# Kernel tuning notes

Hardware: AMD Instinct MI355X
Metric: run time of the kernel (lower is better)

Reference implementation:

```python
import jax, jax.numpy as jnp
import numpy as np

B, L, H, E = 8, 1024, 8, 64
HIST = 512


def setup_inputs() -> dict:
    key = jax.random.key(0)
    ks = jax.random.split(key, 6)
    shp = (B, L, H, E)
    q, k, v, qd, kd, vd = (jax.random.normal(kk, shp, dtype=jnp.float32) for kk in ks)
    # DoubleTriangularCausalMask surrogate: strictly-upper-triangular causal mask (diagonal=1)
    attn_mask = jnp.triu(jnp.ones((L, L), dtype=bool), k=1)[None, None]  # (1,1,L,S)
    return {
        "queries": q, "keys": k, "values": v,
        "queries_drawn": qd, "keys_drawn": kd, "values_drawn": vd,
        "attn_mask": attn_mask, "history_len": HIST,
    }


def reference(queries, keys, values, queries_drawn, keys_drawn, values_drawn, attn_mask, history_len):
    # drawn_y=True branch of FullFixedTimeCausalConstructiveAttention with history_len set.
    B, L, H, E = queries.shape
    scale = 1.0 / float(np.sqrt(E))
    hist = history_len
    idx = jnp.arange(hist, L)

    # queries[:, hist:] = queries_drawn[:, hist:]
    q_eff = jnp.concatenate([queries[:, :hist], queries_drawn[:, hist:]], axis=1)

    scores = jnp.einsum('blhe,bshe->bhls', q_eff, keys)  # (B,H,L,S)
    # diagonal positions l>=hist use drawn keys: q_eff[l] . keys_drawn[l]
    diag_scores = jnp.einsum('blhe,blhe->bhl', q_eff[:, hist:], keys_drawn[:, hist:])
    scores = scores.at[:, :, idx, idx].set(diag_scores)

    scores = jnp.where(attn_mask, -jnp.inf, scores)
    A = jax.nn.softmax(scale * scores, axis=-1)  # (B,H,L,S); dropout rate 0 in eval

    # values substitution on the diagonal (l==s, l>=hist) is a rank-1 correction;
    # avoids materializing the torch (B,H,D,L,S) repeated tensor.
    V = jnp.einsum('bhls,bshd->blhd', A, values)
    diag_A = A[:, :, idx, idx]                      # (B,H,L-hist)
    delta = values_drawn[:, hist:] - values[:, hist:]  # (B,L-hist,H,D)
    V = V.at[:, hist:].add(jnp.transpose(diag_A, (0, 2, 1))[..., None] * delta)
    return V
```

## Files before the change

kernel.cpp:

```cpp
#include <hip/hip_runtime.h>

#define LL   1024
#define HH   8
#define EE   64
#define KSTR 72

#define SCALE2 0.18033688011112043f
#define FMAX8  8.0f

typedef _Float16 f16;
typedef _Float16 v8h  __attribute__((ext_vector_type(8)));
typedef _Float16 h2   __attribute__((ext_vector_type(2)));
typedef float    v4f  __attribute__((ext_vector_type(4)));
typedef int      v2i  __attribute__((ext_vector_type(2)));

__device__ __forceinline__ float fexp2(float x) {
#if __has_builtin(__builtin_amdgcn_exp2f)
  return __builtin_amdgcn_exp2f(x);
#else
  return __expf(x * 0.6931471805599453f);
#endif
}

__device__ __forceinline__ h2 pkh2(float a, float b) {
#if __has_builtin(__builtin_amdgcn_cvt_pkrtz)
  return __builtin_bit_cast(h2, __builtin_amdgcn_cvt_pkrtz(a, b));
#else
  h2 r; r[0] = (f16)a; r[1] = (f16)b; return r;
#endif
}

__device__ __forceinline__ float red4sum(float x) {
#if __has_builtin(__builtin_amdgcn_permlane16_swap) && __has_builtin(__builtin_amdgcn_permlane32_swap)
  int xi = __float_as_int(x);
  v2i a = __builtin_amdgcn_permlane16_swap(xi, xi, false, false);
  float s = __int_as_float(a.x) + __int_as_float(a.y);
  int si = __float_as_int(s);
  v2i b = __builtin_amdgcn_permlane32_swap(si, si, false, false);
  return __int_as_float(b.x) + __int_as_float(b.y);
#else
  x += __shfl_xor(x, 16);
  return x + __shfl_xor(x, 32);
#endif
}

__device__ __forceinline__ void load16f(const float* __restrict__ p, float* __restrict__ f) {
  const float4* p4 = reinterpret_cast<const float4*>(p);
  float4 a = p4[0], b = p4[1], c = p4[2], d = p4[3];
  f[0]=a.x;  f[1]=a.y;  f[2]=a.z;  f[3]=a.w;
  f[4]=b.x;  f[5]=b.y;  f[6]=b.z;  f[7]=b.w;
  f[8]=c.x;  f[9]=c.y;  f[10]=c.z; f[11]=c.w;
  f[12]=d.x; f[13]=d.y; f[14]=d.z; f[15]=d.w;
}

__device__ __forceinline__ void load8f(const float* __restrict__ p, float* __restrict__ f) {
  const float4* p4 = reinterpret_cast<const float4*>(p);
  float4 a = p4[0], b = p4[1];
  f[0]=a.x; f[1]=a.y; f[2]=a.z; f[3]=a.w;
  f[4]=b.x; f[5]=b.y; f[6]=b.z; f[7]=b.w;
}

struct TileState {
  v4f   o[4];
  float l, pd;
};

__device__ __forceinline__ void tile_update(
    TileState& st, const v8h* __restrict__ qf, bool dt, bool drawn,
    const f16* __restrict__ Ks, const f16* __restrict__ Vt,
    const float* __restrict__ zd,
    int w, int ln, int lq,
    const int* __restrict__ rk, const int* __restrict__ kb)
{
  v4f S[4];
#pragma unroll
  for (int nb = 0; nb < 4; ++nb) {
    const f16* krow = &Ks[rk[nb] * KSTR + 8 * lq];
    v8h k0 = *reinterpret_cast<const v8h*>(krow);
    v8h k1 = *reinterpret_cast<const v8h*>(krow + 32);
    v4f acc = (v4f){0.f, 0.f, 0.f, 0.f};
    acc = __builtin_amdgcn_mfma_f32_16x16x32_f16(k0, qf[0], acc, 0, 0, 0);
    acc = __builtin_amdgcn_mfma_f32_16x16x32_f16(k1, qf[1], acc, 0, 0, 0);
    S[nb] = acc;
  }

  const int qlocal = w * 16 + ln;
  float z[4][4];
#pragma unroll
  for (int nb = 0; nb < 4; ++nb)
#pragma unroll
    for (int r = 0; r < 4; ++r) z[nb][r] = S[nb][r] * SCALE2 - FMAX8;

  if (dt) {
    const float zdq = drawn ? (zd[qlocal] - FMAX8) : 0.f;
#pragma unroll
    for (int nb = 0; nb < 4; ++nb) {
#pragma unroll
      for (int r = 0; r < 4; ++r) {
        const int kl = kb[nb] + r;
        if (kl > qlocal)                 z[nb][r] = -1e30f;
        else if (drawn && kl == qlocal)  z[nb][r] = zdq;
      }
    }
  }

  float p[4][4], lsum = 0.f, pdl = 0.f;
#pragma unroll
  for (int nb = 0; nb < 4; ++nb) {
#pragma unroll
    for (int r = 0; r < 4; ++r) {
      const float pv = fexp2(z[nb][r]);
      p[nb][r] = pv;
      lsum += pv;
      if (dt && drawn && (kb[nb] + r) == qlocal) pdl = pv;
    }
  }
  st.l += lsum;
  if (dt && drawn) st.pd = pdl;

  h2 wq[4][2];
#pragma unroll
  for (int nb = 0; nb < 4; ++nb) {
    wq[nb][0] = pkh2(p[nb][0], p[nb][1]);
    wq[nb][1] = pkh2(p[nb][2], p[nb][3]);
  }
  const bool swp = (lq & 1);
  union U8 { v8h v; h2 h[4]; } A0, A1;
  A0.h[0] = swp ? wq[1][0] : wq[0][0];
  A0.h[1] = swp ? wq[1][1] : wq[0][1];
  A0.h[2] = swp ? wq[0][0] : wq[1][0];
  A0.h[3] = swp ? wq[0][1] : wq[1][1];
  A1.h[0] = swp ? wq[3][0] : wq[2][0];
  A1.h[1] = swp ? wq[3][1] : wq[2][1];
  A1.h[2] = swp ? wq[2][0] : wq[3][0];
  A1.h[3] = swp ? wq[2][1] : wq[3][1];

#pragma unroll
  for (int nb = 0; nb < 4; ++nb) {
    const int d   = nb * 16 + ln;
    const int dsw = (d >> 3) & 7;
    const f16* vbase = &Vt[d * KSTR];
    v8h v0 = *reinterpret_cast<const v8h*>(vbase + (((lq    ) ^ dsw) & 7) * 8);
    v8h v1 = *reinterpret_cast<const v8h*>(vbase + (((lq + 4) ^ dsw) & 7) * 8);
    st.o[nb] = __builtin_amdgcn_mfma_f32_16x16x32_f16(v0, A0.v, st.o[nb], 0, 0, 0);
    st.o[nb] = __builtin_amdgcn_mfma_f32_16x16x32_f16(v1, A1.v, st.o[nb], 0, 0, 0);
  }
}

extern "C" __global__ __launch_bounds__(256, 4)
void ftcca_fm(const float* __restrict__ Q,  const float* __restrict__ K,
              const float* __restrict__ V,  const float* __restrict__ Qd,
              const float* __restrict__ Kd, const float* __restrict__ Vd,
              float* __restrict__ out)
{
  __shared__ f16   Ks[64 * KSTR];
  __shared__ f16   Vt[64 * KSTR];
  __shared__ float zdiag[64];

  const int bh  = blockIdx.x & 63;
  const int a   = blockIdx.x >> 6;
  const int qt  = 15 - a;
  const bool drawn = (qt >= 8);
  const int b   = bh >> 3, h = bh & 7;
  const int t   = threadIdx.x;
  const int w    = t >> 6;
  const int lane = t & 63;
  const int ln   = lane & 15;
  const int lq   = lane >> 4;
  const int rs   = t >> 2;
  const int es0  = (t & 3) * 16;
  const int vr0  = (t >> 3) * 2;
  const int vd0  = (t & 7) * 8;

  const size_t base = ((size_t)b * LL * HH + h) * EE;
  const int ROWF = HH * EE;

  const int q2 = ln >> 2;
  int rk[4], kb[4];
  rk[0] = ln + ((q2 + 1) >> 1) * 8;
  rk[1] = ln + 4 + (q2 >> 1) * 8;
  rk[2] = rk[0] + 32;
  rk[3] = rk[1] + 32;
  kb[0] = 4 * lq + ((lq + 1) >> 1) * 8;
  kb[1] = 4 * lq + 4 + (lq >> 1) * 8;
  kb[2] = kb[0] + 32;
  kb[3] = kb[1] + 32;

  if (drawn) {
    const int l = qt * 64 + rs;
    const float* qrow = Qd + base + (size_t)l * ROWF + es0;
    const float* krow = Kd + base + (size_t)l * ROWF + es0;
    float par = 0.f;
#pragma unroll
    for (int i = 0; i < 16; ++i) par += qrow[i] * krow[i];
    par += __shfl_xor(par, 1);
    par += __shfl_xor(par, 2);
    if ((t & 3) == 0) zdiag[rs] = SCALE2 * par;
  }

  const int rowt_q = w * 16 + ln;
  const float* qsrc = drawn ? Qd : Q;
  v8h qf[2];
  {
    const float* pq = qsrc + base + (size_t)(qt * 64 + rowt_q) * ROWF;
#pragma unroll
    for (int c = 0; c < 2; ++c) {
      const float* x = pq + 32 * c + 8 * lq;
#pragma unroll
      for (int j = 0; j < 8; ++j) qf[c][j] = (f16)x[j];
    }
  }

  TileState st;
#pragma unroll
  for (int nb = 0; nb < 4; ++nb) st.o[nb] = (v4f){0, 0, 0, 0};
  st.l = 0.f; st.pd = 0.f;

  float tk[16], tv[16];
  load16f(K + base + (size_t)rs * ROWF + es0, tk);
  load8f(V + base + (size_t)vr0 * ROWF + vd0, tv);
  load8f(V + base + (size_t)(vr0 + 1) * ROWF + vd0, tv + 8);

  for (int i = 0; i <= qt; ++i) {
    __syncthreads();
    {
      v8h k0, k1;
#pragma unroll
      for (int j = 0; j < 8; ++j) { k0[j] = (f16)tk[j]; k1[j] = (f16)tk[8 + j]; }
      v8h* kd0 = reinterpret_cast<v8h*>(&Ks[rs * KSTR + es0]);
      kd0[0] = k0;
      kd0[1] = k1;
      const int vswz = vr0 >> 3;
#pragma unroll
      for (int dd = 0; dd < 8; ++dd) {
        const int d  = vd0 + dd;
        const int ch = (vswz ^ (d >> 3)) & 7;
        h2 val; val[0] = (f16)tv[dd]; val[1] = (f16)tv[8 + dd];
        *reinterpret_cast<h2*>(&Vt[d * KSTR + ch * 8 + (vr0 & 7)]) = val;
      }
    }
    __syncthreads();

    if (i < qt) {
      const size_t r0 = (size_t)((i + 1) * 64);
      load16f(K + base + (r0 + rs) * ROWF + es0, tk);
      load8f(V + base + (r0 + vr0) * ROWF + vd0, tv);
      load8f(V + base + (r0 + vr0 + 1) * ROWF + vd0, tv + 8);
    }

    tile_update(st, qf, i == qt, drawn, Ks, Vt, zdiag, w, ln, lq, rk, kb);
  }

  const float lt = red4sum(st.l);
  const float inv = 1.f / lt;
  const float pdinv = drawn ? (red4sum(st.pd) * inv) : 0.f;
  const int lrow = qt * 64 + w * 16 + ln;

#pragma unroll
  for (int nb = 0; nb < 4; ++nb) {
    const int d0 = nb * 16 + lq * 4;
    const size_t g = base + (size_t)lrow * ROWF + d0;
    float4 o4;
    o4.x = st.o[nb][0] * inv;
    o4.y = st.o[nb][1] * inv;
    o4.z = st.o[nb][2] * inv;
    o4.w = st.o[nb][3] * inv;
    if (drawn) {
      float4 vd4 = *reinterpret_cast<const float4*>(Vd + g);
      float4 v4  = *reinterpret_cast<const float4*>(V + g);
      o4.x += pdinv * (vd4.x - v4.x);
      o4.y += pdinv * (vd4.y - v4.y);
      o4.z += pdinv * (vd4.z - v4.z);
      o4.w += pdinv * (vd4.w - v4.w);
    }
    *reinterpret_cast<float4*>(out + g) = o4;
  }
}

extern "C" void kernel_launch(void* const* d_in, const int* in_sizes, int n_in,
                              void* d_out, int out_size, void* d_ws, size_t ws_size,
                              hipStream_t stream) {
  const float* q  = (const float*)d_in[0];
  const float* k  = (const float*)d_in[1];
  const float* v  = (const float*)d_in[2];
  const float* qd = (const float*)d_in[3];
  const float* kd = (const float*)d_in[4];
  const float* vd = (const float*)d_in[5];
  float* out = (float*)d_out;

  ftcca_fm<<<dim3(1024), dim3(256), 0, stream>>>(q, k, v, qd, kd, vd, out);
}
```

Baseline: 155.1 us.

## Split key tile across wave pairs with 32-row query groups and LDS reduction

Each wave now handles 32 query rows (two 16-row groups) against half of the 64-key tile instead of 16 rows against all keys. Each K and V fragment loaded from LDS feeds two MFMAs, roughly halving LDS reads per MFMA. The partial outputs, row sums and diagonal probabilities of the two key-halves are combined through shared memory at the end. The cost is more registers (launch bounds lowered from 4 to 3 blocks per SM), extra LDS for the reduction buffers, and an added barrier and epilogue pass.

```diff
diff --git a/kernel.cpp b/kernel.cpp
--- a/kernel.cpp
+++ b/kernel.cpp
@@ -3,7 +3,8 @@
 #define LL   1024
 #define HH   8
 #define EE   64
-#define KSTR 72
+#define KSTR  72
+#define OMSTR 68
 
 #define SCALE2 0.18033688011112043f
 #define FMAX8  8.0f
@@ -12,7 +13,8 @@
 typedef _Float16 v8h  __attribute__((ext_vector_type(8)));
 typedef _Float16 h2   __attribute__((ext_vector_type(2)));
 typedef float    v4f  __attribute__((ext_vector_type(4)));
-typedef int      v2i  __attribute__((ext_vector_type(2)));
+
+union U8 { v8h v; h2 hh[4]; };
 
 __device__ __forceinline__ float fexp2(float x) {
 #if __has_builtin(__builtin_amdgcn_exp2f)
@@ -27,20 +29,6 @@
   return __builtin_bit_cast(h2, __builtin_amdgcn_cvt_pkrtz(a, b));
 #else
   h2 r; r[0] = (f16)a; r[1] = (f16)b; return r;
-#endif
-}
-
-__device__ __forceinline__ float red4sum(float x) {
-#if __has_builtin(__builtin_amdgcn_permlane16_swap) && __has_builtin(__builtin_amdgcn_permlane32_swap)
-  int xi = __float_as_int(x);
-  v2i a = __builtin_amdgcn_permlane16_swap(xi, xi, false, false);
-  float s = __int_as_float(a.x) + __int_as_float(a.y);
-  int si = __float_as_int(s);
-  v2i b = __builtin_amdgcn_permlane32_swap(si, si, false, false);
-  return __int_as_float(b.x) + __int_as_float(b.y);
-#else
-  x += __shfl_xor(x, 16);
-  return x + __shfl_xor(x, 32);
 #endif
 }
 
@@ -60,95 +48,8 @@
   f[4]=b.x; f[5]=b.y; f[6]=b.z; f[7]=b.w;
 }
 
-struct TileState {
-  v4f   o[4];
-  float l, pd;
-};
-
-__device__ __forceinline__ void tile_update(
-    TileState& st, const v8h* __restrict__ qf, bool dt, bool drawn,
-    const f16* __restrict__ Ks, const f16* __restrict__ Vt,
-    const float* __restrict__ zd,
-    int w, int ln, int lq,
-    const int* __restrict__ rk, const int* __restrict__ kb)
-{
-  v4f S[4];
-#pragma unroll
-  for (int nb = 0; nb < 4; ++nb) {
-    const f16* krow = &Ks[rk[nb] * KSTR + 8 * lq];
-    v8h k0 = *reinterpret_cast<const v8h*>(krow);
-    v8h k1 = *reinterpret_cast<const v8h*>(krow + 32);
-    v4f acc = (v4f){0.f, 0.f, 0.f, 0.f};
-    acc = __builtin_amdgcn_mfma_f32_16x16x32_f16(k0, qf[0], acc, 0, 0, 0);
-    acc = __builtin_amdgcn_mfma_f32_16x16x32_f16(k1, qf[1], acc, 0, 0, 0);
-    S[nb] = acc;
-  }
-
-  const int qlocal = w * 16 + ln;
-  float z[4][4];
-#pragma unroll
-  for (int nb = 0; nb < 4; ++nb)
-#pragma unroll
-    for (int r = 0; r < 4; ++r) z[nb][r] = S[nb][r] * SCALE2 - FMAX8;
-
-  if (dt) {
-    const float zdq = drawn ? (zd[qlocal] - FMAX8) : 0.f;
-#pragma unroll
-    for (int nb = 0; nb < 4; ++nb) {
-#pragma unroll
-      for (int r = 0; r < 4; ++r) {
-        const int kl = kb[nb] + r;
-        if (kl > qlocal)                 z[nb][r] = -1e30f;
-        else if (drawn && kl == qlocal)  z[nb][r] = zdq;
-      }
-    }
-  }
-
-  float p[4][4], lsum = 0.f, pdl = 0.f;
-#pragma unroll
-  for (int nb = 0; nb < 4; ++nb) {
-#pragma unroll
-    for (int r = 0; r < 4; ++r) {
-      const float pv = fexp2(z[nb][r]);
-      p[nb][r] = pv;
-      lsum += pv;
-      if (dt && drawn && (kb[nb] + r) == qlocal) pdl = pv;
-    }
-  }
-  st.l += lsum;
-  if (dt && drawn) st.pd = pdl;
-
-  h2 wq[4][2];
-#pragma unroll
-  for (int nb = 0; nb < 4; ++nb) {
-    wq[nb][0] = pkh2(p[nb][0], p[nb][1]);
-    wq[nb][1] = pkh2(p[nb][2], p[nb][3]);
-  }
-  const bool swp = (lq & 1);
-  union U8 { v8h v; h2 h[4]; } A0, A1;
-  A0.h[0] = swp ? wq[1][0] : wq[0][0];
-  A0.h[1] = swp ? wq[1][1] : wq[0][1];
-  A0.h[2] = swp ? wq[0][0] : wq[1][0];
-  A0.h[3] = swp ? wq[0][1] : wq[1][1];
-  A1.h[0] = swp ? wq[3][0] : wq[2][0];
-  A1.h[1] = swp ? wq[3][1] : wq[2][1];
-  A1.h[2] = swp ? wq[2][0] : wq[3][0];
-  A1.h[3] = swp ? wq[2][1] : wq[3][1];
-
-#pragma unroll
-  for (int nb = 0; nb < 4; ++nb) {
-    const int d   = nb * 16 + ln;
-    const int dsw = (d >> 3) & 7;
-    const f16* vbase = &Vt[d * KSTR];
-    v8h v0 = *reinterpret_cast<const v8h*>(vbase + (((lq    ) ^ dsw) & 7) * 8);
-    v8h v1 = *reinterpret_cast<const v8h*>(vbase + (((lq + 4) ^ dsw) & 7) * 8);
-    st.o[nb] = __builtin_amdgcn_mfma_f32_16x16x32_f16(v0, A0.v, st.o[nb], 0, 0, 0);
-    st.o[nb] = __builtin_amdgcn_mfma_f32_16x16x32_f16(v1, A1.v, st.o[nb], 0, 0, 0);
-  }
-}
-
-extern "C" __global__ __launch_bounds__(256, 4)
-void ftcca_fm(const float* __restrict__ Q,  const float* __restrict__ K,
+extern "C" __global__ __launch_bounds__(256, 3)
+void ftcca_ws(const float* __restrict__ Q,  const float* __restrict__ K,
               const float* __restrict__ V,  const float* __restrict__ Qd,
               const float* __restrict__ Kd, const float* __restrict__ Vd,
               float* __restrict__ out)
@@ -156,6 +57,9 @@
   __shared__ f16   Ks[64 * KSTR];
   __shared__ f16   Vt[64 * KSTR];
   __shared__ float zdiag[64];
+  __shared__ float Om[2][32 * OMSTR];
+  __shared__ float lbuf[64][9];
+  __shared__ float pdbuf[64][9];
 
   const int bh  = blockIdx.x & 63;
   const int a   = blockIdx.x >> 6;
@@ -163,7 +67,9 @@
   const bool drawn = (qt >= 8);
   const int b   = bh >> 3, h = bh & 7;
   const int t   = threadIdx.x;
-  const int w    = t >> 6;
+  const int wid = t >> 6;
+  const int wq  = wid >> 1;
+  const int ws  = wid & 1;
   const int lane = t & 63;
   const int ln   = lane & 15;
   const int lq   = lane >> 4;
@@ -176,15 +82,10 @@
   const int ROWF = HH * EE;
 
   const int q2 = ln >> 2;
-  int rk[4], kb[4];
-  rk[0] = ln + ((q2 + 1) >> 1) * 8;
-  rk[1] = ln + 4 + (q2 >> 1) * 8;
-  rk[2] = rk[0] + 32;
-  rk[3] = rk[1] + 32;
-  kb[0] = 4 * lq + ((lq + 1) >> 1) * 8;
-  kb[1] = 4 * lq + 4 + (lq >> 1) * 8;
-  kb[2] = kb[0] + 32;
-  kb[3] = kb[1] + 32;
+  const int rk0 = ln + ((q2 + 1) >> 1) * 8;
+  const int rk1 = ln + 4 + (q2 >> 1) * 8;
+  const int kb0 = 4 * lq + ((lq + 1) >> 1) * 8;
+  const int kb1 = 4 * lq + 4 + (lq >> 1) * 8;
 
   if (drawn) {
     const int l = qt * 64 + rs;
@@ -198,23 +99,24 @@
     if ((t & 3) == 0) zdiag[rs] = SCALE2 * par;
   }
 
-  const int rowt_q = w * 16 + ln;
   const float* qsrc = drawn ? Qd : Q;
-  v8h qf[2];
-  {
-    const float* pq = qsrc + base + (size_t)(qt * 64 + rowt_q) * ROWF;
+  v8h qf[2][2];
+#pragma unroll
+  for (int g = 0; g < 2; ++g) {
+    const float* pq = qsrc + base + (size_t)(qt * 64 + 32 * wq + 16 * g + ln) * ROWF;
 #pragma unroll
     for (int c = 0; c < 2; ++c) {
       const float* x = pq + 32 * c + 8 * lq;
 #pragma unroll
-      for (int j = 0; j < 8; ++j) qf[c][j] = (f16)x[j];
-    }
-  }
-
-  TileState st;
-#pragma unroll
-  for (int nb = 0; nb < 4; ++nb) st.o[nb] = (v4f){0, 0, 0, 0};
-  st.l = 0.f; st.pd = 0.f;
+      for (int j = 0; j < 8; ++j) qf[g][c][j] = (f16)x[j];
+    }
+  }
+
+  v4f o[4][2];
+#pragma unroll
+  for (int nd = 0; nd < 4; ++nd) { o[nd][0] = (v4f){0,0,0,0}; o[nd][1] = (v4f){0,0,0,0}; }
+  float lacc[2] = {0.f, 0.f};
+  float pdacc[2] = {0.f, 0.f};
 
   float tk[16], tv[16];
   load16f(K + base + (size_t)rs * ROWF + es0, tk);
@@ -248,32 +150,128 @@
       load8f(V + base + (r0 + vr0 + 1) * ROWF + vd0, tv + 8);
     }
 
-    tile_update(st, qf, i == qt, drawn, Ks, Vt, zdiag, w, ln, lq, rk, kb);
-  }
-
-  const float lt = red4sum(st.l);
-  const float inv = 1.f / lt;
-  const float pdinv = drawn ? (red4sum(st.pd) * inv) : 0.f;
-  const int lrow = qt * 64 + w * 16 + ln;
-
-#pragma unroll
-  for (int nb = 0; nb < 4; ++nb) {
-    const int d0 = nb * 16 + lq * 4;
-    const size_t g = base + (size_t)lrow * ROWF + d0;
-    float4 o4;
-    o4.x = st.o[nb][0] * inv;
-    o4.y = st.o[nb][1] * inv;
-    o4.z = st.o[nb][2] * inv;
-    o4.w = st.o[nb][3] * inv;
-    if (drawn) {
-      float4 vd4 = *reinterpret_cast<const float4*>(Vd + g);
-      float4 v4  = *reinterpret_cast<const float4*>(V + g);
-      o4.x += pdinv * (vd4.x - v4.x);
-      o4.y += pdinv * (vd4.y - v4.y);
-      o4.z += pdinv * (vd4.z - v4.z);
-      o4.w += pdinv * (vd4.w - v4.w);
-    }
-    *reinterpret_cast<float4*>(out + g) = o4;
+    const bool dt = (i == qt);
+
+    const f16* kr0 = &Ks[(32 * ws + rk0) * KSTR + 8 * lq];
+    const f16* kr1 = &Ks[(32 * ws + rk1) * KSTR + 8 * lq];
+    v8h a00 = *reinterpret_cast<const v8h*>(kr0);
+    v8h a01 = *reinterpret_cast<const v8h*>(kr0 + 32);
+    v8h a10 = *reinterpret_cast<const v8h*>(kr1);
+    v8h a11 = *reinterpret_cast<const v8h*>(kr1 + 32);
+
+    U8 Bf[2];
+#pragma unroll
+    for (int g = 0; g < 2; ++g) {
+      v4f S0 = (v4f){0,0,0,0}, S1 = (v4f){0,0,0,0};
+      S0 = __builtin_amdgcn_mfma_f32_16x16x32_f16(a00, qf[g][0], S0, 0, 0, 0);
+      S0 = __builtin_amdgcn_mfma_f32_16x16x32_f16(a01, qf[g][1], S0, 0, 0, 0);
+      S1 = __builtin_amdgcn_mfma_f32_16x16x32_f16(a10, qf[g][0], S1, 0, 0, 0);
+      S1 = __builtin_amdgcn_mfma_f32_16x16x32_f16(a11, qf[g][1], S1, 0, 0, 0);
+
+      const int ql = 32 * wq + 16 * g + ln;
+      const float zdq = (dt && drawn) ? (zdiag[ql] - FMAX8) : 0.f;
+
+      float p0[4], p1[4], ls = 0.f, pdl = 0.f;
+#pragma unroll
+      for (int r = 0; r < 4; ++r) {
+        float z0 = S0[r] * SCALE2 - FMAX8;
+        float z1 = S1[r] * SCALE2 - FMAX8;
+        if (dt) {
+          const int kl0 = 32 * ws + kb0 + r;
+          const int kl1 = 32 * ws + kb1 + r;
+          if (kl0 > ql)                 z0 = -1e30f;
+          else if (drawn && kl0 == ql)  z0 = zdq;
+          if (kl1 > ql)                 z1 = -1e30f;
+          else if (drawn && kl1 == ql)  z1 = zdq;
+        }
+        const float pv0 = fexp2(z0);
+        const float pv1 = fexp2(z1);
+        p0[r] = pv0; p1[r] = pv1;
+        ls += pv0 + pv1;
+        if (dt && drawn) {
+          if ((32 * ws + kb0 + r) == ql) pdl += pv0;
+          if ((32 * ws + kb1 + r) == ql) pdl += pv1;
+        }
+      }
+      lacc[g] += ls;
+      pdacc[g] += pdl;
+
+      const h2 pkA = pkh2(p0[0], p0[1]);
+      const h2 pkB = pkh2(p0[2], p0[3]);
+      const h2 pkC = pkh2(p1[0], p1[1]);
+      const h2 pkD = pkh2(p1[2], p1[3]);
+      const bool swp = (lq & 1);
+      Bf[g].hh[0] = swp ? pkC : pkA;
+      Bf[g].hh[1] = swp ? pkD : pkB;
+      Bf[g].hh[2] = swp ? pkA : pkC;
+      Bf[g].hh[3] = swp ? pkB : pkD;
+    }
+
+#pragma unroll
+    for (int nd = 0; nd < 4; ++nd) {
+      const int d   = nd * 16 + ln;
+      const int dsw = (d >> 3) & 7;
+      const int ch  = ((4 * ws + lq) ^ dsw) & 7;
+      v8h vf = *reinterpret_cast<const v8h*>(&Vt[d * KSTR + ch * 8]);
+      o[nd][0] = __builtin_amdgcn_mfma_f32_16x16x32_f16(vf, Bf[0].v, o[nd][0], 0, 0, 0);
+      o[nd][1] = __builtin_amdgcn_mfma_f32_16x16x32_f16(vf, Bf[1].v, o[nd][1], 0, 0, 0);
+    }
+  }
+
+#pragma unroll
+  for (int g = 0; g < 2; ++g) {
+    const int ql = 32 * wq + 16 * g + ln;
+    lbuf[ql][lq + 4 * ws]  = lacc[g];
+    pdbuf[ql][lq + 4 * ws] = pdacc[g];
+  }
+  if (ws == 1) {
+#pragma unroll
+    for (int nd = 0; nd < 4; ++nd)
+#pragma unroll
+      for (int g = 0; g < 2; ++g) {
+        float4 o4;
+        o4.x = o[nd][g][0]; o4.y = o[nd][g][1]; o4.z = o[nd][g][2]; o4.w = o[nd][g][3];
+        *reinterpret_cast<float4*>(&Om[wq][(16 * g + ln) * OMSTR + 16 * nd + 4 * lq]) = o4;
+      }
+  }
+  __syncthreads();
+  if (ws == 0) {
+#pragma unroll
+    for (int g = 0; g < 2; ++g) {
+      const int ql = 32 * wq + 16 * g + ln;
+      float lt = 0.f;
+#pragma unroll
+      for (int j = 0; j < 8; ++j) lt += lbuf[ql][j];
+      const float inv = 1.f / lt;
+      float pdinv = 0.f;
+      if (drawn) {
+        float pdv = 0.f;
+#pragma unroll
+        for (int j = 0; j < 8; ++j) pdv += pdbuf[ql][j];
+        pdinv = pdv * inv;
+      }
+      const int lrow = qt * 64 + ql;
+#pragma unroll
+      for (int nd = 0; nd < 4; ++nd) {
+        const int d0 = nd * 16 + 4 * lq;
+        const size_t gaddr = base + (size_t)lrow * ROWF + d0;
+        float4 ob = *reinterpret_cast<const float4*>(&Om[wq][(16 * g + ln) * OMSTR + 16 * nd + 4 * lq]);
+        float4 o4;
+        o4.x = (o[nd][g][0] + ob.x) * inv;
+        o4.y = (o[nd][g][1] + ob.y) * inv;
+        o4.z = (o[nd][g][2] + ob.z) * inv;
+        o4.w = (o[nd][g][3] + ob.w) * inv;
+        if (drawn) {
+          float4 vd4 = *reinterpret_cast<const float4*>(Vd + gaddr);
+          float4 v4  = *reinterpret_cast<const float4*>(V + gaddr);
+          o4.x += pdinv * (vd4.x - v4.x);
+          o4.y += pdinv * (vd4.y - v4.y);
+          o4.z += pdinv * (vd4.z - v4.z);
+          o4.w += pdinv * (vd4.w - v4.w);
+        }
+        *reinterpret_cast<float4*>(out + gaddr) = o4;
+      }
+    }
   }
 }
 
@@ -288,5 +286,5 @@
   const float* vd = (const float*)d_in[5];
   float* out = (float*)d_out;
 
-  ftcca_fm<<<dim3(1024), dim3(256), 0, stream>>>(q, k, v, qd, kd, vd, out);
-}
+  ftcca_ws<<<dim3(1024), dim3(256), 0, stream>>>(q, k, v, qd, kd, vd, out);
+}
```

After: 155.0 us. No clear change (-0.1%).
